# Kernel tuning notes

Hardware: AMD Instinct MI355X
Metric: run time of the kernel (lower is better)

The kernel has to match this reference:

```python
import jax, jax.numpy as jnp
import numpy as np

B, T, D, H, E, K = 4, 2048, 512, 1024, 8, 2


def setup_inputs() -> dict:
    key = jax.random.key(0)
    ks = jax.random.split(key, 6)
    x = jax.random.normal(ks[0], (B, T, D), dtype=jnp.float32)
    Wg = jax.random.normal(ks[1], (D, E), dtype=jnp.float32) / np.sqrt(D)  # gate (no bias)
    W1 = jax.random.normal(ks[2], (E, D, H), dtype=jnp.float32) / np.sqrt(D)
    b1 = jnp.zeros((E, H), dtype=jnp.float32)
    W2 = jax.random.normal(ks[3], (E, H, D), dtype=jnp.float32) / np.sqrt(H)
    b2 = jnp.zeros((E, D), dtype=jnp.float32)
    return {"x": x, "Wg": Wg, "W1": W1, "b1": b1, "W2": W2, "b2": b2}


def reference(x, Wg, W1, b1, W2, b2):
    # Dropout is identity at inference (p applied only in train mode).
    Bx, Tx, Dx = x.shape
    N = Bx * Tx
    xf = x.reshape(N, Dx)

    # --- Router: top-k over gate logits, softmax over the k selected logits ---
    router_logits = xf @ Wg                               # [N, E]
    topk_logits, topk_idx = jax.lax.top_k(router_logits, K)  # [N, K]
    topk_w = jax.nn.softmax(topk_logits, axis=-1)         # [N, K]

    # Dense combine weights: combine[n, e] = sum of topk weights routing token n to expert e
    combine = jnp.zeros((N, E), dtype=x.dtype).at[
        jnp.arange(N)[:, None], topk_idx
    ].add(topk_w)                                         # [N, E]

    # --- Experts (batched over E): GELU(x W1 + b1) W2 + b2 ---
    h = jax.nn.gelu(jnp.einsum('nd,edh->enh', xf, W1) + b1[:, None, :],
                    approximate=False)                    # [E, N, H]
    y = jnp.einsum('enh,ehd->end', h, W2) + b2[:, None, :]  # [E, N, D]

    # --- Combine: weighted sum of expert outputs per token ---
    out = jnp.einsum('end,ne->nd', y, combine).reshape(Bx, Tx, Dx)

    aux_logits = router_logits.reshape(Bx, Tx, E)
    aux_idx = topk_idx.reshape(Bx, Tx, K)
    aux_w = topk_w.reshape(Bx, Tx, K)
    return out, aux_logits, aux_idx, aux_w
```

## Files before the change

### kernel.cpp

```cpp
#include <hip/hip_runtime.h>
#include <hip/hip_bf16.h>

#define NTOK 8192
#define DDIM 512
#define HDIM 1024
#define NEXP 8
#define TOPK 2

typedef __attribute__((ext_vector_type(8))) short short8;
typedef __attribute__((ext_vector_type(4))) float f32x4;

__device__ __forceinline__ short f2bf(float f) {
  union { float f; unsigned u; } v; v.f = f;
  unsigned r = v.u + 0x7fffu + ((v.u >> 16) & 1u);
  return (short)(r >> 16);
}
__device__ __forceinline__ float bf2f(short s) {
  union { unsigned u; float f; } v; v.u = ((unsigned)(unsigned short)s) << 16;
  return v.f;
}

__device__ __forceinline__ void async_lds16(const void* g, void* l) {
  __builtin_amdgcn_global_load_lds(
      (const __attribute__((address_space(1))) unsigned int*)g,
      (__attribute__((address_space(3))) unsigned int*)l,
      16, 0, 0);
}

__device__ __forceinline__ float gelu_f(float v) {
  float u2 = v * v;
  float z = v * (-1.5957691216f - 0.0713548163f * u2);
  float t = __expf(z);
  return v * __builtin_amdgcn_rcpf(1.f + t);
}

__global__ __launch_bounds__(256) void transpose_bf16_kernel(const float* __restrict__ src,
                                                             short* __restrict__ dst,
                                                             int R, int C) {
  __shared__ float tile[32][33];
  int m = blockIdx.z;
  int c0 = blockIdx.x * 32, r0 = blockIdx.y * 32;
  const float* s = src + (size_t)m * R * C;
  short* d = dst + (size_t)m * R * C;
  int tx = threadIdx.x, ty = threadIdx.y;
#pragma unroll
  for (int i = 0; i < 4; ++i)
    tile[ty + i * 8][tx] = s[(size_t)(r0 + ty + i * 8) * C + c0 + tx];
  __syncthreads();
#pragma unroll
  for (int i = 0; i < 4; ++i)
    d[(size_t)(c0 + ty + i * 8) * R + r0 + tx] = f2bf(tile[tx][ty + i * 8]);
}

__global__ __launch_bounds__(256) void router_compute(
    const float* __restrict__ x, const float* __restrict__ wg,
    float* __restrict__ out_logits, float* __restrict__ out_idx,
    float* __restrict__ out_w, short* __restrict__ xb) {
  int wave = threadIdx.x >> 6;
  int lane = threadIdx.x & 63;
  int n = blockIdx.x * 4 + wave;

  const float* xrow = x + (size_t)n * DDIM;
  const float4* xv = (const float4*)xrow;
  float4 xa = xv[lane * 2], xbv = xv[lane * 2 + 1];
  float xs[8] = {xa.x, xa.y, xa.z, xa.w, xbv.x, xbv.y, xbv.z, xbv.w};

  short8 xc;
#pragma unroll
  for (int j = 0; j < 8; ++j) xc[j] = f2bf(xs[j]);
  *(short8*)(xb + (size_t)n * DDIM + lane * 8) = xc;

  float acc[8] = {0, 0, 0, 0, 0, 0, 0, 0};
#pragma unroll
  for (int j = 0; j < 8; ++j) {
    const float4* wr = (const float4*)(wg + (size_t)(lane * 8 + j) * NEXP);
    float4 w0 = wr[0], w1 = wr[1];
    float xj = xs[j];
    acc[0] += xj * w0.x; acc[1] += xj * w0.y; acc[2] += xj * w0.z; acc[3] += xj * w0.w;
    acc[4] += xj * w1.x; acc[5] += xj * w1.y; acc[6] += xj * w1.z; acc[7] += xj * w1.w;
  }
#pragma unroll
  for (int m = 32; m >= 1; m >>= 1) {
#pragma unroll
    for (int e = 0; e < 8; ++e) acc[e] += __shfl_xor(acc[e], m);
  }
  if (lane == 0) {
#pragma unroll
    for (int e = 0; e < 8; ++e) out_logits[(size_t)n * NEXP + e] = acc[e];
    int i1 = 0; float v1 = acc[0];
#pragma unroll
    for (int e = 1; e < 8; ++e) if (acc[e] > v1) { v1 = acc[e]; i1 = e; }
    int i2 = -1; float v2 = -3.4e38f;
#pragma unroll
    for (int e = 0; e < 8; ++e) if (e != i1 && acc[e] > v2) { v2 = acc[e]; i2 = e; }
    float ex = expf(v2 - v1);
    float s = 1.f / (1.f + ex);
    out_idx[n * 2] = (float)i1; out_idx[n * 2 + 1] = (float)i2;
    out_w[n * 2] = s; out_w[n * 2 + 1] = ex * s;
  }
}

__global__ __launch_bounds__(512) void build_lists(
    const float* __restrict__ idxf,
    int* __restrict__ counts, int* __restrict__ tok_list, int* __restrict__ slot_enc) {
  int t = blockIdx.x * 512 + threadIdx.x;
  int lane = threadIdx.x & 63;
  float2 iv = *(const float2*)(idxf + (size_t)t * 2);
  int es[2] = {(int)iv.x, (int)iv.y};
#pragma unroll
  for (int s = 0; s < 2; ++s) {
    int e = es[s];
#pragma unroll
    for (int ex = 0; ex < NEXP; ++ex) {
      unsigned long long m = __ballot(e == ex);
      if (e == ex) {
        int leader = __ffsll(m) - 1;
        int base = 0;
        if (lane == leader) base = atomicAdd(&counts[ex], __popcll(m));
        base = __shfl(base, leader);
        int rank = __popcll(m & ((1ull << lane) - 1ull));
        tok_list[ex * NTOK + base + rank] = t;
        slot_enc[t * 2 + s] = (ex << 16) | (base + rank);
      }
    }
  }
}

__global__ __launch_bounds__(256) void expert_gemm1(
    const short* __restrict__ xb, const short* __restrict__ w1t,
    const float* __restrict__ b1, short* __restrict__ hbuf,
    const int* __restrict__ ctrl, const int* __restrict__ tok_list) {
  int raw = blockIdx.x;
  int bid = (raw & 7) * 512 + (raw >> 3);
  int e = bid >> 9;
  int rem = bid & 511;
  int mt = rem >> 3;
  int nt = rem & 7;
  int ce = ctrl[e];
  int m0 = mt * 128;
  if (m0 >= ce) return;
  int offe = 0;
#pragma unroll
  for (int i = 0; i < NEXP; ++i) offe += (i < e) ? ctrl[i] : 0;

  __shared__ char smem[49152];

  int tid = threadIdx.x;
  int wave = tid >> 6;
  int lane = tid & 63;

  int sr = tid >> 2;
  int kc = (((tid & 3) ^ ((sr >> 1) & 3)) * 8);
  int ia = m0 + sr;      if (ia >= ce) ia = ce - 1;
  int ib = m0 + sr + 64; if (ib >= ce) ib = ce - 1;
  const short* gA0 = xb + (size_t)tok_list[e * NTOK + ia] * DDIM + kc;
  const short* gA1 = xb + (size_t)tok_list[e * NTOK + ib] * DDIM + kc;
  const short* gB0 = w1t + ((size_t)e * HDIM + nt * 128 + sr) * DDIM + kc;
  const short* gB1 = gB0 + (size_t)64 * DDIM;

  f32x4 acc[4][4];
#pragma unroll
  for (int i = 0; i < 4; ++i)
#pragma unroll
    for (int j = 0; j < 4; ++j) acc[i][j] = (f32x4){0.f, 0.f, 0.f, 0.f};

  int wm = (wave >> 1) * 64;
  int wn = (wave & 1) * 64;
  int lr = lane & 15;
  int kswz = ((lane >> 4) * 8) ^ (((lr >> 1) & 3) << 3);

#define STAGE1(t) do {                                                  \
    int _k = (t) * 32;                                                  \
    char* _lA = smem + ((t) % 3) * 16384 + wave * 1024;                 \
    char* _lB = _lA + 8192;                                             \
    async_lds16(gA0 + _k, _lA); async_lds16(gA1 + _k, _lA + 4096);      \
    async_lds16(gB0 + _k, _lB); async_lds16(gB1 + _k, _lB + 4096);      \
  } while (0)

  STAGE1(0);
  STAGE1(1);
#pragma unroll
  for (int t = 0; t < 16; ++t) {
    if (t < 15) asm volatile("s_waitcnt vmcnt(4)\n\ts_barrier" ::: "memory");
    else        asm volatile("s_waitcnt vmcnt(0)\n\ts_barrier" ::: "memory");
    __builtin_amdgcn_sched_barrier(0);
    if (t + 2 < 16) STAGE1(t + 2);
    const short* As = (const short*)(smem + (t % 3) * 16384);
    const short* Bs = As + 4096;
    short8 a[4], b[4];
#pragma unroll
    for (int i = 0; i < 4; ++i) a[i] = *(const short8*)&As[(wm + i * 16 + lr) * 32 + kswz];
#pragma unroll
    for (int j = 0; j < 4; ++j) b[j] = *(const short8*)&Bs[(wn + j * 16 + lr) * 32 + kswz];
    asm volatile("s_waitcnt lgkmcnt(0)" ::: "memory");
    __builtin_amdgcn_sched_barrier(0);
    __builtin_amdgcn_s_setprio(1);
#pragma unroll
    for (int i = 0; i < 4; ++i)
#pragma unroll
      for (int j = 0; j < 4; ++j)
        acc[i][j] = __builtin_amdgcn_mfma_f32_16x16x32_bf16(a[i], b[j], acc[i][j], 0, 0, 0);
    __builtin_amdgcn_s_setprio(0);
  }
#undef STAGE1
  __syncthreads();

  short* ep = (short*)(smem + wave * 8704);
  int colb = nt * 128 + wn;
#pragma unroll
  for (int j = 0; j < 4; ++j) {
    int colH = colb + j * 16 + lr;
    float bb = b1[e * HDIM + colH];
#pragma unroll
    for (int i = 0; i < 4; ++i) {
#pragma unroll
      for (int q = 0; q < 4; ++q) {
        int rl = i * 16 + (lane >> 4) * 4 + q;
        ep[rl * 68 + j * 16 + lr] = f2bf(gelu_f(acc[i][j][q] + bb));
      }
    }
  }
  __syncthreads();
#pragma unroll
  for (int s = 0; s < 8; ++s) {
    int idx = s * 64 + lane;
    int rl = idx >> 3;
    int c8 = (idx & 7) * 8;
    int gidx = m0 + wm + rl;
    if (gidx < ce) {
      *(short8*)&hbuf[(size_t)(offe + gidx) * HDIM + colb + c8] = *(short8*)&ep[rl * 68 + c8];
    }
  }
}

__global__ __launch_bounds__(256) void expert_gemm2(
    const short* __restrict__ hbuf, const short* __restrict__ w2t,
    const float* __restrict__ b2, short* __restrict__ ybuf,
    const int* __restrict__ ctrl) {
  int raw = blockIdx.x;
  int bid = (raw & 7) * 256 + (raw >> 3);
  int e = bid >> 8;
  int rem = bid & 255;
  int mt = rem >> 2;
  int nt = rem & 3;
  int ce = ctrl[e];
  int m0 = mt * 128;
  if (m0 >= ce) return;
  int offe = 0;
#pragma unroll
  for (int i = 0; i < NEXP; ++i) offe += (i < e) ? ctrl[i] : 0;

  __shared__ char smem[49152];

  int tid = threadIdx.x;
  int wave = tid >> 6;
  int lane = tid & 63;

  int sr = tid >> 2;
  int kc = (((tid & 3) ^ ((sr >> 1) & 3)) * 8);
  int ia = m0 + sr;      if (ia >= ce) ia = ce - 1;
  int ib = m0 + sr + 64; if (ib >= ce) ib = ce - 1;
  const short* gA0 = hbuf + (size_t)(offe + ia) * HDIM + kc;
  const short* gA1 = hbuf + (size_t)(offe + ib) * HDIM + kc;
  const short* gB0 = w2t + ((size_t)e * DDIM + nt * 128 + sr) * HDIM + kc;
  const short* gB1 = gB0 + (size_t)64 * HDIM;

  f32x4 acc[4][4];
#pragma unroll
  for (int i = 0; i < 4; ++i)
#pragma unroll
    for (int j = 0; j < 4; ++j) acc[i][j] = (f32x4){0.f, 0.f, 0.f, 0.f};

  int wm = (wave >> 1) * 64;
  int wn = (wave & 1) * 64;
  int lr = lane & 15;
  int kswz = ((lane >> 4) * 8) ^ (((lr >> 1) & 3) << 3);

#define STAGE2(t) do {                                                  \
    int _k = (t) * 32;                                                  \
    char* _lA = smem + ((t) % 3) * 16384 + wave * 1024;                 \
    char* _lB = _lA + 8192;                                             \
    async_lds16(gA0 + _k, _lA); async_lds16(gA1 + _k, _lA + 4096);      \
    async_lds16(gB0 + _k, _lB); async_lds16(gB1 + _k, _lB + 4096);      \
  } while (0)

  STAGE2(0);
  STAGE2(1);
#pragma unroll
  for (int t = 0; t < 32; ++t) {
    if (t < 31) asm volatile("s_waitcnt vmcnt(4)\n\ts_barrier" ::: "memory");
    else        asm volatile("s_waitcnt vmcnt(0)\n\ts_barrier" ::: "memory");
    __builtin_amdgcn_sched_barrier(0);
    if (t + 2 < 32) STAGE2(t + 2);
    const short* As = (const short*)(smem + (t % 3) * 16384);
    const short* Bs = As + 4096;
    short8 a[4], b[4];
#pragma unroll
    for (int i = 0; i < 4; ++i) a[i] = *(const short8*)&As[(wm + i * 16 + lr) * 32 + kswz];
#pragma unroll
    for (int j = 0; j < 4; ++j) b[j] = *(const short8*)&Bs[(wn + j * 16 + lr) * 32 + kswz];
    asm volatile("s_waitcnt lgkmcnt(0)" ::: "memory");
    __builtin_amdgcn_sched_barrier(0);
    __builtin_amdgcn_s_setprio(1);
#pragma unroll
    for (int i = 0; i < 4; ++i)
#pragma unroll
      for (int j = 0; j < 4; ++j)
        acc[i][j] = __builtin_amdgcn_mfma_f32_16x16x32_bf16(a[i], b[j], acc[i][j], 0, 0, 0);
    __builtin_amdgcn_s_setprio(0);
  }
#undef STAGE2
  __syncthreads();

  short* ep = (short*)(smem + wave * 8704);
  int colb = nt * 128 + wn;
#pragma unroll
  for (int j = 0; j < 4; ++j) {
    int colD = colb + j * 16 + lr;
    float bb = b2[e * DDIM + colD];
#pragma unroll
    for (int i = 0; i < 4; ++i) {
#pragma unroll
      for (int q = 0; q < 4; ++q) {
        int rl = i * 16 + (lane >> 4) * 4 + q;
        ep[rl * 68 + j * 16 + lr] = f2bf(acc[i][j][q] + bb);
      }
    }
  }
  __syncthreads();
#pragma unroll
  for (int s = 0; s < 8; ++s) {
    int idx = s * 64 + lane;
    int rl = idx >> 3;
    int c8 = (idx & 7) * 8;
    int gidx = m0 + wm + rl;
    if (gidx < ce) {
      *(short8*)&ybuf[(size_t)(offe + gidx) * DDIM + colb + c8] = *(short8*)&ep[rl * 68 + c8];
    }
  }
}

__global__ __launch_bounds__(256) void combine_kernel(
    const short* __restrict__ ybuf, const int* __restrict__ slot_enc,
    const float* __restrict__ wf, const int* __restrict__ ctrl,
    float* __restrict__ out) {
  int wave = threadIdx.x >> 6;
  int lane = threadIdx.x & 63;
  int n = blockIdx.x * 4 + wave;
  int s0 = slot_enc[n * 2], s1 = slot_enc[n * 2 + 1];
  float w0 = wf[n * 2], w1 = wf[n * 2 + 1];
  int e0 = s0 >> 16, e1 = s1 >> 16;
  int off0 = 0, off1 = 0;
#pragma unroll
  for (int i = 0; i < NEXP; ++i) {
    int c = ctrl[i];
    off0 += (i < e0) ? c : 0;
    off1 += (i < e1) ? c : 0;
  }
  int r0 = off0 + (s0 & 0xffff);
  int r1 = off1 + (s1 & 0xffff);
  short8 a = *(const short8*)&ybuf[(size_t)r0 * DDIM + lane * 8];
  short8 b = *(const short8*)&ybuf[(size_t)r1 * DDIM + lane * 8];
  float r[8];
#pragma unroll
  for (int k = 0; k < 8; ++k) r[k] = w0 * bf2f(a[k]) + w1 * bf2f(b[k]);
  float4 o0 = {r[0], r[1], r[2], r[3]};
  float4 o1 = {r[4], r[5], r[6], r[7]};
  *(float4*)&out[(size_t)n * DDIM + lane * 8] = o0;
  *(float4*)&out[(size_t)n * DDIM + lane * 8 + 4] = o1;
}

extern "C" void kernel_launch(void* const* d_in, const int* in_sizes, int n_in,
                              void* d_out, int out_size, void* d_ws, size_t ws_size,
                              hipStream_t stream) {
  const float* x  = (const float*)d_in[0];
  const float* wg = (const float*)d_in[1];
  const float* w1 = (const float*)d_in[2];
  const float* b1 = (const float*)d_in[3];
  const float* w2 = (const float*)d_in[4];
  const float* b2 = (const float*)d_in[5];
  float* out = (float*)d_out;

  char* ws = (char*)d_ws;
  int*   ctrl = (int*)ws;
  int*   tok  = (int*)(ws + 1024);
  int*   slot = (int*)(ws + 263168);
  short* xb   = (short*)(ws + 328704);
  short* w1t  = (short*)(ws + 8717312);
  short* w2t  = (short*)(ws + 17105920);
  short* hb   = (short*)(ws + 25494528);
  short* yb   = (short*)(ws + 328704);

  hipMemsetAsync(d_ws, 0, 1024, stream);

  transpose_bf16_kernel<<<dim3(32, 16, 8), dim3(32, 8), 0, stream>>>(w1, w1t, DDIM, HDIM);
  transpose_bf16_kernel<<<dim3(16, 32, 8), dim3(32, 8), 0, stream>>>(w2, w2t, HDIM, DDIM);

  float* out_logits = out + (size_t)NTOK * DDIM;
  float* out_idx = out_logits + (size_t)NTOK * NEXP;
  float* out_w = out_idx + (size_t)NTOK * TOPK;
  router_compute<<<2048, 256, 0, stream>>>(x, wg, out_logits, out_idx, out_w, xb);
  build_lists<<<16, 512, 0, stream>>>(out_idx, ctrl, tok, slot);

  expert_gemm1<<<4096, 256, 0, stream>>>(xb, w1t, b1, hb, ctrl, tok);
  expert_gemm2<<<2048, 256, 0, stream>>>(hb, w2t, b2, yb, ctrl);
  combine_kernel<<<2048, 256, 0, stream>>>(yb, slot, out_w, ctrl, out);
}
```

Before: 133.6 us.

## Enlarge expert GEMM tiles to 256x256 with 8 waves and double buffering

Both expert GEMMs move from 128x128 tiles with 4 waves and triple-buffered LDS to 256x256 tiles with 8 waves (512 threads), each wave computing 128x64 via 8x4 MFMA accumulators. LDS goes to two 32KB buffers with a full vmcnt(0) wait per K step, and the epilogue is staged in four 32-row passes to fit. The separate memset of the expert counters is dropped and the counters are zeroed inside the router kernel instead. Larger tiles raise operand reuse per loaded byte but cut the grid to far fewer blocks and double accumulator register pressure. Waiting for all loads each step also reduces how much load latency is overlapped with compute.

```diff
diff --git a/kernel.cpp b/kernel.cpp
--- a/kernel.cpp
+++ b/kernel.cpp
@@ -55,7 +55,8 @@
 __global__ __launch_bounds__(256) void router_compute(
     const float* __restrict__ x, const float* __restrict__ wg,
     float* __restrict__ out_logits, float* __restrict__ out_idx,
-    float* __restrict__ out_w, short* __restrict__ xb) {
+    float* __restrict__ out_w, short* __restrict__ xb, int* __restrict__ counts) {
+  if (blockIdx.x == 0 && threadIdx.x < NEXP) counts[threadIdx.x] = 0;
   int wave = threadIdx.x >> 6;
   int lane = threadIdx.x & 63;
   int n = blockIdx.x * 4 + wave;
@@ -126,77 +127,80 @@
   }
 }
 
-__global__ __launch_bounds__(256) void expert_gemm1(
+__global__ __launch_bounds__(512, 2) void expert_gemm1(
     const short* __restrict__ xb, const short* __restrict__ w1t,
     const float* __restrict__ b1, short* __restrict__ hbuf,
     const int* __restrict__ ctrl, const int* __restrict__ tok_list) {
   int raw = blockIdx.x;
-  int bid = (raw & 7) * 512 + (raw >> 3);
-  int e = bid >> 9;
-  int rem = bid & 511;
-  int mt = rem >> 3;
-  int nt = rem & 7;
+  int bid = (raw & 7) * 64 + (raw >> 3);
+  int e = bid >> 6;
+  int rem = bid & 63;
+  int mt = rem >> 2;
+  int nt = rem & 3;
   int ce = ctrl[e];
-  int m0 = mt * 128;
+  int m0 = mt * 256;
   if (m0 >= ce) return;
   int offe = 0;
 #pragma unroll
   for (int i = 0; i < NEXP; ++i) offe += (i < e) ? ctrl[i] : 0;
 
-  __shared__ char smem[49152];
+  __shared__ char smem[65536];
 
   int tid = threadIdx.x;
   int wave = tid >> 6;
   int lane = tid & 63;
 
-  int sr = tid >> 2;
-  int kc = (((tid & 3) ^ ((sr >> 1) & 3)) * 8);
-  int ia = m0 + sr;      if (ia >= ce) ia = ce - 1;
-  int ib = m0 + sr + 64; if (ib >= ce) ib = ce - 1;
-  const short* gA0 = xb + (size_t)tok_list[e * NTOK + ia] * DDIM + kc;
-  const short* gA1 = xb + (size_t)tok_list[e * NTOK + ib] * DDIM + kc;
-  const short* gB0 = w1t + ((size_t)e * HDIM + nt * 128 + sr) * DDIM + kc;
-  const short* gB1 = gB0 + (size_t)64 * DDIM;
-
-  f32x4 acc[4][4];
-#pragma unroll
-  for (int i = 0; i < 4; ++i)
+  int laneRow = lane >> 2;
+  int chunk = lane & 3;
+  int r0 = wave * 32 + laneRow;
+  int r1 = r0 + 16;
+  int swz0 = (chunk ^ ((r0 >> 1) & 3)) * 8;
+  int swz1 = (chunk ^ ((r1 >> 1) & 3)) * 8;
+  int ga0 = m0 + r0; if (ga0 >= ce) ga0 = ce - 1;
+  int ga1 = m0 + r1; if (ga1 >= ce) ga1 = ce - 1;
+  const short* a0 = xb + (size_t)tok_list[e * NTOK + ga0] * DDIM + swz0;
+  const short* a1 = xb + (size_t)tok_list[e * NTOK + ga1] * DDIM + swz1;
+  const short* b0 = w1t + ((size_t)e * HDIM + nt * 256 + r0) * DDIM + swz0;
+  const short* b1p = w1t + ((size_t)e * HDIM + nt * 256 + r1) * DDIM + swz1;
+
+  f32x4 acc[8][4];
+#pragma unroll
+  for (int i = 0; i < 8; ++i)
 #pragma unroll
     for (int j = 0; j < 4; ++j) acc[i][j] = (f32x4){0.f, 0.f, 0.f, 0.f};
 
-  int wm = (wave >> 1) * 64;
-  int wn = (wave & 1) * 64;
+  int wm = (wave >> 2) * 128;
+  int wn = (wave & 3) * 64;
   int lr = lane & 15;
   int kswz = ((lane >> 4) * 8) ^ (((lr >> 1) & 3) << 3);
 
-#define STAGE1(t) do {                                                  \
-    int _k = (t) * 32;                                                  \
-    char* _lA = smem + ((t) % 3) * 16384 + wave * 1024;                 \
-    char* _lB = _lA + 8192;                                             \
-    async_lds16(gA0 + _k, _lA); async_lds16(gA1 + _k, _lA + 4096);      \
-    async_lds16(gB0 + _k, _lB); async_lds16(gB1 + _k, _lB + 4096);      \
+#define STAGE1(t) do {                                                   \
+    int _k = (t) * 32;                                                   \
+    char* _b = smem + (((t) & 1) << 15);                                 \
+    async_lds16(a0 + _k, _b + (wave * 32) * 64);                         \
+    async_lds16(a1 + _k, _b + (wave * 32 + 16) * 64);                    \
+    async_lds16(b0 + _k, _b + 16384 + (wave * 32) * 64);                 \
+    async_lds16(b1p + _k, _b + 16384 + (wave * 32 + 16) * 64);           \
   } while (0)
 
   STAGE1(0);
-  STAGE1(1);
 #pragma unroll
   for (int t = 0; t < 16; ++t) {
-    if (t < 15) asm volatile("s_waitcnt vmcnt(4)\n\ts_barrier" ::: "memory");
-    else        asm volatile("s_waitcnt vmcnt(0)\n\ts_barrier" ::: "memory");
+    asm volatile("s_waitcnt vmcnt(0)\n\ts_barrier" ::: "memory");
     __builtin_amdgcn_sched_barrier(0);
-    if (t + 2 < 16) STAGE1(t + 2);
-    const short* As = (const short*)(smem + (t % 3) * 16384);
-    const short* Bs = As + 4096;
-    short8 a[4], b[4];
-#pragma unroll
-    for (int i = 0; i < 4; ++i) a[i] = *(const short8*)&As[(wm + i * 16 + lr) * 32 + kswz];
+    if (t + 1 < 16) STAGE1(t + 1);
+    const short* As = (const short*)(smem + ((t & 1) << 15));
+    const short* Bs = As + 8192;
+    short8 a[8], b[4];
+#pragma unroll
+    for (int i = 0; i < 8; ++i) a[i] = *(const short8*)&As[(wm + i * 16 + lr) * 32 + kswz];
 #pragma unroll
     for (int j = 0; j < 4; ++j) b[j] = *(const short8*)&Bs[(wn + j * 16 + lr) * 32 + kswz];
     asm volatile("s_waitcnt lgkmcnt(0)" ::: "memory");
     __builtin_amdgcn_sched_barrier(0);
     __builtin_amdgcn_s_setprio(1);
 #pragma unroll
-    for (int i = 0; i < 4; ++i)
+    for (int i = 0; i < 8; ++i)
 #pragma unroll
       for (int j = 0; j < 4; ++j)
         acc[i][j] = __builtin_amdgcn_mfma_f32_16x16x32_bf16(a[i], b[j], acc[i][j], 0, 0, 0);
@@ -205,105 +209,114 @@
 #undef STAGE1
   __syncthreads();
 
-  short* ep = (short*)(smem + wave * 8704);
-  int colb = nt * 128 + wn;
-#pragma unroll
-  for (int j = 0; j < 4; ++j) {
-    int colH = colb + j * 16 + lr;
-    float bb = b1[e * HDIM + colH];
-#pragma unroll
-    for (int i = 0; i < 4; ++i) {
-#pragma unroll
-      for (int q = 0; q < 4; ++q) {
-        int rl = i * 16 + (lane >> 4) * 4 + q;
-        ep[rl * 68 + j * 16 + lr] = f2bf(gelu_f(acc[i][j][q] + bb));
+  int colb = nt * 256 + wn;
+  float bb[4];
+#pragma unroll
+  for (int j = 0; j < 4; ++j) bb[j] = b1[e * HDIM + colb + j * 16 + lr];
+  short* ep = (short*)smem + wave * 2176;
+#pragma unroll
+  for (int p = 0; p < 4; ++p) {
+#pragma unroll
+    for (int ii = 0; ii < 2; ++ii) {
+      int i = p * 2 + ii;
+#pragma unroll
+      for (int j = 0; j < 4; ++j) {
+#pragma unroll
+        for (int q = 0; q < 4; ++q) {
+          int rl = ii * 16 + (lane >> 4) * 4 + q;
+          ep[rl * 68 + j * 16 + lr] = f2bf(gelu_f(acc[i][j][q] + bb[j]));
+        }
       }
     }
-  }
-  __syncthreads();
-#pragma unroll
-  for (int s = 0; s < 8; ++s) {
-    int idx = s * 64 + lane;
-    int rl = idx >> 3;
-    int c8 = (idx & 7) * 8;
-    int gidx = m0 + wm + rl;
-    if (gidx < ce) {
-      *(short8*)&hbuf[(size_t)(offe + gidx) * HDIM + colb + c8] = *(short8*)&ep[rl * 68 + c8];
+    __syncthreads();
+#pragma unroll
+    for (int s = 0; s < 4; ++s) {
+      int idx = s * 64 + lane;
+      int rl = idx >> 3;
+      int c8 = (idx & 7) * 8;
+      int gidx = m0 + wm + p * 32 + rl;
+      if (gidx < ce) {
+        *(short8*)&hbuf[(size_t)(offe + gidx) * HDIM + colb + c8] = *(short8*)&ep[rl * 68 + c8];
+      }
     }
-  }
-}
-
-__global__ __launch_bounds__(256) void expert_gemm2(
+    __syncthreads();
+  }
+}
+
+__global__ __launch_bounds__(512, 2) void expert_gemm2(
     const short* __restrict__ hbuf, const short* __restrict__ w2t,
     const float* __restrict__ b2, short* __restrict__ ybuf,
     const int* __restrict__ ctrl) {
   int raw = blockIdx.x;
-  int bid = (raw & 7) * 256 + (raw >> 3);
-  int e = bid >> 8;
-  int rem = bid & 255;
-  int mt = rem >> 2;
-  int nt = rem & 3;
+  int bid = (raw & 7) * 32 + (raw >> 3);
+  int e = bid >> 5;
+  int rem = bid & 31;
+  int mt = rem >> 1;
+  int nt = rem & 1;
   int ce = ctrl[e];
-  int m0 = mt * 128;
+  int m0 = mt * 256;
   if (m0 >= ce) return;
   int offe = 0;
 #pragma unroll
   for (int i = 0; i < NEXP; ++i) offe += (i < e) ? ctrl[i] : 0;
 
-  __shared__ char smem[49152];
+  __shared__ char smem[65536];
 
   int tid = threadIdx.x;
   int wave = tid >> 6;
   int lane = tid & 63;
 
-  int sr = tid >> 2;
-  int kc = (((tid & 3) ^ ((sr >> 1) & 3)) * 8);
-  int ia = m0 + sr;      if (ia >= ce) ia = ce - 1;
-  int ib = m0 + sr + 64; if (ib >= ce) ib = ce - 1;
-  const short* gA0 = hbuf + (size_t)(offe + ia) * HDIM + kc;
-  const short* gA1 = hbuf + (size_t)(offe + ib) * HDIM + kc;
-  const short* gB0 = w2t + ((size_t)e * DDIM + nt * 128 + sr) * HDIM + kc;
-  const short* gB1 = gB0 + (size_t)64 * HDIM;
-
-  f32x4 acc[4][4];
-#pragma unroll
-  for (int i = 0; i < 4; ++i)
+  int laneRow = lane >> 2;
+  int chunk = lane & 3;
+  int r0 = wave * 32 + laneRow;
+  int r1 = r0 + 16;
+  int swz0 = (chunk ^ ((r0 >> 1) & 3)) * 8;
+  int swz1 = (chunk ^ ((r1 >> 1) & 3)) * 8;
+  int ga0 = m0 + r0; if (ga0 >= ce) ga0 = ce - 1;
+  int ga1 = m0 + r1; if (ga1 >= ce) ga1 = ce - 1;
+  const short* a0 = hbuf + (size_t)(offe + ga0) * HDIM + swz0;
+  const short* a1 = hbuf + (size_t)(offe + ga1) * HDIM + swz1;
+  const short* b0 = w2t + ((size_t)e * DDIM + nt * 256 + r0) * HDIM + swz0;
+  const short* b1p = w2t + ((size_t)e * DDIM + nt * 256 + r1) * HDIM + swz1;
+
+  f32x4 acc[8][4];
+#pragma unroll
+  for (int i = 0; i < 8; ++i)
 #pragma unroll
     for (int j = 0; j < 4; ++j) acc[i][j] = (f32x4){0.f, 0.f, 0.f, 0.f};
 
-  int wm = (wave >> 1) * 64;
-  int wn = (wave & 1) * 64;
+  int wm = (wave >> 2) * 128;
+  int wn = (wave & 3) * 64;
   int lr = lane & 15;
   int kswz = ((lane >> 4) * 8) ^ (((lr >> 1) & 3) << 3);
 
-#define STAGE2(t) do {                                                  \
-    int _k = (t) * 32;                                                  \
-    char* _lA = smem + ((t) % 3) * 16384 + wave * 1024;                 \
-    char* _lB = _lA + 8192;                                             \
-    async_lds16(gA0 + _k, _lA); async_lds16(gA1 + _k, _lA + 4096);      \
-    async_lds16(gB0 + _k, _lB); async_lds16(gB1 + _k, _lB + 4096);      \
+#define STAGE2(t) do {                                                   \
+    int _k = (t) * 32;                                                   \
+    char* _b = smem + (((t) & 1) << 15);                                 \
+    async_lds16(a0 + _k, _b + (wave * 32) * 64);                         \
+    async_lds16(a1 + _k, _b + (wave * 32 + 16) * 64);                    \
+    async_lds16(b0 + _k, _b + 16384 + (wave * 32) * 64);                 \
+    async_lds16(b1p + _k, _b + 16384 + (wave * 32 + 16) * 64);           \
   } while (0)
 
   STAGE2(0);
-  STAGE2(1);
 #pragma unroll
   for (int t = 0; t < 32; ++t) {
-    if (t < 31) asm volatile("s_waitcnt vmcnt(4)\n\ts_barrier" ::: "memory");
-    else        asm volatile("s_waitcnt vmcnt(0)\n\ts_barrier" ::: "memory");
+    asm volatile("s_waitcnt vmcnt(0)\n\ts_barrier" ::: "memory");
     __builtin_amdgcn_sched_barrier(0);
-    if (t + 2 < 32) STAGE2(t + 2);
-    const short* As = (const short*)(smem + (t % 3) * 16384);
-    const short* Bs = As + 4096;
-    short8 a[4], b[4];
-#pragma unroll
-    for (int i = 0; i < 4; ++i) a[i] = *(const short8*)&As[(wm + i * 16 + lr) * 32 + kswz];
+    if (t + 1 < 32) STAGE2(t + 1);
+    const short* As = (const short*)(smem + ((t & 1) << 15));
+    const short* Bs = As + 8192;
+    short8 a[8], b[4];
+#pragma unroll
+    for (int i = 0; i < 8; ++i) a[i] = *(const short8*)&As[(wm + i * 16 + lr) * 32 + kswz];
 #pragma unroll
     for (int j = 0; j < 4; ++j) b[j] = *(const short8*)&Bs[(wn + j * 16 + lr) * 32 + kswz];
     asm volatile("s_waitcnt lgkmcnt(0)" ::: "memory");
     __builtin_amdgcn_sched_barrier(0);
     __builtin_amdgcn_s_setprio(1);
 #pragma unroll
-    for (int i = 0; i < 4; ++i)
+    for (int i = 0; i < 8; ++i)
 #pragma unroll
       for (int j = 0; j < 4; ++j)
         acc[i][j] = __builtin_amdgcn_mfma_f32_16x16x32_bf16(a[i], b[j], acc[i][j], 0, 0, 0);
@@ -312,31 +325,37 @@
 #undef STAGE2
   __syncthreads();
 
-  short* ep = (short*)(smem + wave * 8704);
-  int colb = nt * 128 + wn;
-#pragma unroll
-  for (int j = 0; j < 4; ++j) {
-    int colD = colb + j * 16 + lr;
-    float bb = b2[e * DDIM + colD];
-#pragma unroll
-    for (int i = 0; i < 4; ++i) {
-#pragma unroll
-      for (int q = 0; q < 4; ++q) {
-        int rl = i * 16 + (lane >> 4) * 4 + q;
-        ep[rl * 68 + j * 16 + lr] = f2bf(acc[i][j][q] + bb);
+  int colb = nt * 256 + wn;
+  float bb[4];
+#pragma unroll
+  for (int j = 0; j < 4; ++j) bb[j] = b2[e * DDIM + colb + j * 16 + lr];
+  short* ep = (short*)smem + wave * 2176;
+#pragma unroll
+  for (int p = 0; p < 4; ++p) {
+#pragma unroll
+    for (int ii = 0; ii < 2; ++ii) {
+      int i = p * 2 + ii;
+#pragma unroll
+      for (int j = 0; j < 4; ++j) {
+#pragma unroll
+        for (int q = 0; q < 4; ++q) {
+          int rl = ii * 16 + (lane >> 4) * 4 + q;
+          ep[rl * 68 + j * 16 + lr] = f2bf(acc[i][j][q] + bb[j]);
+        }
       }
     }
-  }
-  __syncthreads();
-#pragma unroll
-  for (int s = 0; s < 8; ++s) {
-    int idx = s * 64 + lane;
-    int rl = idx >> 3;
-    int c8 = (idx & 7) * 8;
-    int gidx = m0 + wm + rl;
-    if (gidx < ce) {
-      *(short8*)&ybuf[(size_t)(offe + gidx) * DDIM + colb + c8] = *(short8*)&ep[rl * 68 + c8];
+    __syncthreads();
+#pragma unroll
+    for (int s = 0; s < 4; ++s) {
+      int idx = s * 64 + lane;
+      int rl = idx >> 3;
+      int c8 = (idx & 7) * 8;
+      int gidx = m0 + wm + p * 32 + rl;
+      if (gidx < ce) {
+        *(short8*)&ybuf[(size_t)(offe + gidx) * DDIM + colb + c8] = *(short8*)&ep[rl * 68 + c8];
+      }
     }
+    __syncthreads();
   }
 }
 
@@ -391,18 +410,16 @@
   short* hb   = (short*)(ws + 25494528);
   short* yb   = (short*)(ws + 328704);
 
-  hipMemsetAsync(d_ws, 0, 1024, stream);
-
   transpose_bf16_kernel<<<dim3(32, 16, 8), dim3(32, 8), 0, stream>>>(w1, w1t, DDIM, HDIM);
   transpose_bf16_kernel<<<dim3(16, 32, 8), dim3(32, 8), 0, stream>>>(w2, w2t, HDIM, DDIM);
 
   float* out_logits = out + (size_t)NTOK * DDIM;
   float* out_idx = out_logits + (size_t)NTOK * NEXP;
   float* out_w = out_idx + (size_t)NTOK * TOPK;
-  router_compute<<<2048, 256, 0, stream>>>(x, wg, out_logits, out_idx, out_w, xb);
+  router_compute<<<2048, 256, 0, stream>>>(x, wg, out_logits, out_idx, out_w, xb, ctrl);
   build_lists<<<16, 512, 0, stream>>>(out_idx, ctrl, tok, slot);
 
-  expert_gemm1<<<4096, 256, 0, stream>>>(xb, w1t, b1, hb, ctrl, tok);
-  expert_gemm2<<<2048, 256, 0, stream>>>(hb, w2t, b2, yb, ctrl);
+  expert_gemm1<<<512, 512, 0, stream>>>(xb, w1t, b1, hb, ctrl, tok);
+  expert_gemm2<<<256, 512, 0, stream>>>(hb, w2t, b2, yb, ctrl);
   combine_kernel<<<2048, 256, 0, stream>>>(yb, slot, out_w, ctrl, out);
 }
```

Result: slower. 143.8 us (+7.6%).
